# Kernel tuning notes

Measured on AMD Instinct MI355X. Metric: run time of the kernel, lower is better.

Reference implementation:

```python
import jax, jax.numpy as jnp
import numpy as np

N, D, NCLS = 1, 64, 21
R, C = 512, 512
R_IN, C_IN = 256, 256


def setup_inputs() -> dict:
    key = jax.random.key(0)
    k1, k2, k3 = jax.random.split(key, 3)
    # regular mesh with unit spacing -> grid_interval_X = grid_interval_Y = 1.0
    gy, gx = jnp.meshgrid(jnp.arange(R, dtype=jnp.float32),
                          jnp.arange(C, dtype=jnp.float32), indexing='ij')
    grid = jnp.stack([gy, gx], axis=-1)[None]  # [1,R,C,2]
    # float query coordinates inside the grid
    u = jax.random.uniform(k1, (N, R_IN, C_IN, 2), dtype=jnp.float32)
    grid_inte = u * jnp.array([R - 1.0, C - 1.0], dtype=jnp.float32)
    feat = jax.random.normal(k2, (N, D, R_IN, C_IN), dtype=jnp.float32)
    lbs = jax.random.uniform(k3, (N, NCLS, R, C), dtype=jnp.float32)
    wei = jnp.float32(1.0)
    return {"grid_inte": grid_inte, "grid": grid, "feat": feat, "lbs": lbs, "wei": wei}


def _forward(grid_inte, grid, feat, lbs, wei):
    n, r_in, c_in, _ = grid_inte.shape
    r, c = grid.shape[1], grid.shape[2]
    d = feat.shape[1]
    ncls = lbs.shape[1]
    M = r_in * c_in

    dx = grid[0, 2, 2, 0] - grid[0, 1, 2, 0]
    dy = grid[0, 2, 2, 1] - grid[0, 2, 1, 1]

    # bilinear upsample feat (half-pixel centers, matches torch align_corners=False)
    feat_grid = jax.image.resize(feat, (n, d, r, c), method='bilinear')
    feat_grid = feat_grid.reshape(d, r * c)              # N == 1

    # integer cell indices of each query (no grad, as in torch.no_grad())
    rp0 = jax.lax.stop_gradient(jnp.floor(grid_inte[..., 0] / dx)).astype(jnp.int32).reshape(-1)
    rp1 = jax.lax.stop_gradient(jnp.floor(grid_inte[..., 1] / dy)).astype(jnp.int32).reshape(-1)

    offs = jnp.arange(-2, 3, dtype=jnp.int32)
    oi, oj = jnp.meshgrid(offs, offs, indexing='ij')     # 5x5 neighborhood
    oi, oj = oi.reshape(-1), oj.reshape(-1)              # [25]
    rows = jnp.clip(rp0[None, :] + oi[:, None], 0, r - 1)  # [25, M]
    cols = jnp.clip(rp1[None, :] + oj[:, None], 0, c - 1)
    idx = rows * c + cols                                 # [25, M]

    fg = feat_grid[:, idx]                                # [D, 25, M] gather
    feat_flat = feat.reshape(d, M)
    # Gaussian-style affinity per tap: exp(-wei * mean_D (diff^2))
    dist = jnp.exp(-wei * jnp.mean((fg - feat_flat[:, None, :]) ** 2, axis=0))  # [25, M]

    lbs_flat = lbs.reshape(ncls, r * c)
    lg = lbs_flat[:, idx]                                 # [ncls, 25, M] gather
    voting = jnp.einsum('ctm,tm->cm', lg, dist)           # weighted label voting
    dist_sum = jnp.sum(dist, axis=0)                      # [M]
    out = voting / jnp.clip(dist_sum, 1e-15)[None, :]
    return out.reshape(n, ncls, r_in, c_in)


def reference(grid_inte, grid, feat, lbs, wei):
    return _forward(grid_inte, grid, feat, lbs, wei)
```

## Files before the change

### kernel.cpp

```cpp
#include <hip/hip_runtime.h>
#include <stdint.h>

#define M_TOT 65536
#define LBS_S 262144
#define REC   24

typedef _Float16 h2 __attribute__((ext_vector_type(2)));
typedef _Float16 h8 __attribute__((ext_vector_type(8)));
typedef float fx2 __attribute__((ext_vector_type(2)));
union H8 { h8 v; h2 h[4]; };

__device__ __forceinline__ int rfl(int v) { return __builtin_amdgcn_readfirstlane(v); }
__device__ __forceinline__ float bperm(int l, float v) {
  return __int_as_float(__builtin_amdgcn_ds_bpermute(l << 2, __float_as_int(v)));
}
__device__ __forceinline__ int bpermi(int l, int v) {
  return __builtin_amdgcn_ds_bpermute(l << 2, v);
}
__device__ __forceinline__ float merge2(float a, float b, bool hi, int xo) {
  const float keep = hi ? b : a;
  const float send = hi ? a : b;
  return keep + __shfl_xor(send, xo, 64);
}

#if __has_builtin(__builtin_amdgcn_fdot2)
__device__ __forceinline__ float fdot2(h2 a, h2 b, float c) {
  return __builtin_amdgcn_fdot2(a, b, c, false);
}
#else
__device__ __forceinline__ float fdot2(h2 a, h2 b, float c) {
  return fmaf((float)a.x, (float)b.x, fmaf((float)a.y, (float)b.y, c));
}
#endif

#if __has_builtin(__builtin_amdgcn_cvt_pk_f32_fp8) && __has_builtin(__builtin_amdgcn_cvt_pk_fp8_f32)
#define FP8_HW 1
#endif

__device__ __forceinline__ uint32_t enc1_sw(float x) {
  uint32_t b = __float_as_uint(x);
  const uint32_t s = b >> 31;
  uint32_t ax = b & 0x7fffffffu;
  if (ax > 0x43e00000u) ax = 0x43e00000u;
  const int e = (int)(ax >> 23) - 127;
  uint32_t out;
  if (e >= -6) {
    const uint32_t r = ax + 0x00080000u;
    const int e2 = (int)(r >> 23) - 127;
    if (e2 > 8) out = (15u << 3) | 6u;
    else out = ((uint32_t)(e2 + 7) << 3) | ((r >> 20) & 7u);
  } else if (e >= -10) {
    const float af = __uint_as_float(ax);
    int m = (int)(af * 512.0f + 0.5f);
    out = (m > 7) ? ((1u << 3) | 0u) : (uint32_t)m;
  } else {
    out = 0;
  }
  return out | (s << 7);
}
__device__ __forceinline__ float dec1_sw(uint32_t b) {
  const uint32_t e = (b >> 3) & 15u, m = b & 7u;
  float f;
  if (e) f = __uint_as_float(((e + 120u) << 23) | (m << 20));
  else f = (float)m * 0.001953125f;
  return (b & 0x80u) ? -f : f;
}

__device__ __forceinline__ uint32_t enc_pk4(float a, float b, float c, float d) {
#ifdef FP8_HW
  int r = __builtin_amdgcn_cvt_pk_fp8_f32(a, b, 0, false);
  r = __builtin_amdgcn_cvt_pk_fp8_f32(c, d, r, true);
  return (uint32_t)r;
#else
  return enc1_sw(a) | (enc1_sw(b) << 8) | (enc1_sw(c) << 16) | (enc1_sw(d) << 24);
#endif
}
__device__ __forceinline__ void dec_pk8(uint32_t lo, uint32_t hi, float* o) {
#ifdef FP8_HW
  const fx2 a = __builtin_amdgcn_cvt_pk_f32_fp8((int)lo, false);
  const fx2 b = __builtin_amdgcn_cvt_pk_f32_fp8((int)lo, true);
  const fx2 c = __builtin_amdgcn_cvt_pk_f32_fp8((int)hi, false);
  const fx2 d = __builtin_amdgcn_cvt_pk_f32_fp8((int)hi, true);
  o[0] = a.x; o[1] = a.y; o[2] = b.x; o[3] = b.y;
  o[4] = c.x; o[5] = c.y; o[6] = d.x; o[7] = d.y;
#else
  o[0] = dec1_sw(lo & 255); o[1] = dec1_sw((lo >> 8) & 255);
  o[2] = dec1_sw((lo >> 16) & 255); o[3] = dec1_sw(lo >> 24);
  o[4] = dec1_sw(hi & 255); o[5] = dec1_sw((hi >> 8) & 255);
  o[6] = dec1_sw((hi >> 16) & 255); o[7] = dec1_sw(hi >> 24);
#endif
}

__global__ __launch_bounds__(256) void k_prep(const float* __restrict__ feat,
                                              const float* __restrict__ lbs,
                                              _Float16* __restrict__ feat_h,
                                              uint8_t* __restrict__ feat_q,
                                              uint8_t* __restrict__ rec) {
  __shared__ float ldsf[64 * 65];
  const int l = threadIdx.x & 63;
  const int w = threadIdx.x >> 6;
  if (blockIdx.x < 1024) {
    float(*tile)[65] = (float(*)[65])ldsf;
    const int s0 = blockIdx.x * 64;
#pragma unroll
    for (int k = 0; k < 16; ++k) {
      const int d = w * 16 + k;
      tile[d][l] = feat[(size_t)d * M_TOT + s0 + l];
    }
    __syncthreads();
    const int lh = l & 31, hs = l >> 5;
    h2* out2 = (h2*)feat_h;
#pragma unroll
    for (int k = 0; k < 8; ++k) {
      const int s = w * 16 + 2 * k + hs;
      h2 v;
      v.x = (_Float16)tile[2 * lh][s];
      v.y = (_Float16)tile[2 * lh + 1][s];
      out2[(size_t)(s0 + s) * 32 + lh] = v;
    }
    uint2* outq = (uint2*)feat_q;
#pragma unroll
    for (int it = 0; it < 2; ++it) {
      const int s = w * 16 + it * 8 + (l >> 3);
      const int cb = l & 7;
      const float* col = &tile[8 * cb][s];
      uint2 u;
      u.x = enc_pk4(col[0 * 65], col[1 * 65], col[2 * 65], col[3 * 65]);
      u.y = enc_pk4(col[4 * 65], col[5 * 65], col[6 * 65], col[7 * 65]);
      outq[(size_t)(s0 + s) * 8 + cb] = u;
    }
  } else {
    uint8_t* buf = ((uint8_t*)ldsf) + w * (64 * REC);
    const int sb = (blockIdx.x - 1024) * 256 + w * 64;
#pragma unroll
    for (int c = 0; c < 21; ++c)
      buf[l * REC + 2 + c] = (uint8_t)(lbs[(size_t)c * LBS_S + sb + l] * 255.0f + 0.5f);
    __syncthreads();
    const uint32_t* src = (const uint32_t*)buf;
    uint32_t* dst = (uint32_t*)(rec + (size_t)sb * REC);
#pragma unroll
    for (int k = 0; k < 6; ++k) dst[k * 64 + l] = src[k * 64 + l];
  }
}

__global__ __launch_bounds__(256) void k_n2(const uint8_t* __restrict__ feat_q,
                                            uint8_t* __restrict__ rec) {
  const int lane = threadIdx.x & 63;
  const int cb = lane & 7;
  const int g = lane >> 3;
  const int quad = blockIdx.x * 32 + (int)(threadIdx.x >> 6) * 8 + g;
  const int a = quad >> 8;
  const int b = quad & 255;
  const int ra[3] = {max(a - 1, 0), a, min(a + 1, 255)};
  const int cbn[3] = {max(b - 1, 0), b, min(b + 1, 255)};

  const uint2* fq = (const uint2*)feat_q;
  float F[3][3][8];
#pragma unroll
  for (int i = 0; i < 3; ++i)
#pragma unroll
    for (int j = 0; j < 3; ++j) {
      const uint2 u = fq[(size_t)((ra[i] << 8) + cbn[j]) * 8 + cb];
      dec_pk8(u.x, u.y, F[i][j]);
    }

  float wye[2], wxe[2];
  int cye[2], cxe[2];
#pragma unroll
  for (int e = 0; e < 2; ++e) {
    const float yf = fminf(fmaxf((float)(2 * a + e) * 0.5f - 0.25f, 0.0f), 255.0f);
    const int y0 = min((int)yf, 254);
    wye[e] = yf - (float)y0;
    cye[e] = y0 - (a - 1);
    const float xf = fminf(fmaxf((float)(2 * b + e) * 0.5f - 0.25f, 0.0f), 255.0f);
    const int x0 = min((int)xf, 254);
    wxe[e] = xf - (float)x0;
    cxe[e] = x0 - (b - 1);
  }

  float colv[3][2][8];
#pragma unroll
  for (int r = 0; r < 3; ++r)
#pragma unroll
    for (int e = 0; e < 2; ++e) {
      const bool s1 = (cxe[e] == 1);
#pragma unroll
      for (int j = 0; j < 8; ++j) {
        const float A = s1 ? F[r][1][j] : F[r][0][j];
        const float B = s1 ? F[r][2][j] : F[r][1][j];
        colv[r][e][j] = fmaf(wxe[e], B - A, A);
      }
    }

  float sq[4];
#pragma unroll
  for (int ey = 0; ey < 2; ++ey)
#pragma unroll
    for (int ex = 0; ex < 2; ++ex) {
      const bool s1 = (cye[ey] == 1);
      float nn = 0.0f;
#pragma unroll
      for (int j = 0; j < 8; ++j) {
        const float A = s1 ? colv[1][ex][j] : colv[0][ex][j];
        const float B = s1 ? colv[2][ex][j] : colv[1][ex][j];
        const float v = fmaf(wye[ey], B - A, A);
        nn = fmaf(v, v, nn);
      }
      sq[ey * 2 + ex] = nn;
    }

  const bool b0 = lane & 1, b1 = lane & 2;
  float m0 = merge2(sq[0], sq[1], b0, 1);
  float m1 = merge2(sq[2], sq[3], b0, 1);
  float mm = merge2(m0, m1, b1, 2);
  mm += __shfl_xor(mm, 4, 64);
  if ((lane & 7) < 4) {
    const int ey = (lane >> 1) & 1, ex = lane & 1;
    *(_Float16*)(rec + (size_t)((2 * a + ey) * 512 + 2 * b + ex) * REC) = (_Float16)mm;
  }
}

__global__ __launch_bounds__(256) void k_main(const float* __restrict__ grid_inte,
                                              const float* __restrict__ grid,
                                              const _Float16* __restrict__ feat_h,
                                              const uint8_t* __restrict__ feat_q,
                                              const uint8_t* __restrict__ rec,
                                              const float* __restrict__ wei_p,
                                              float* __restrict__ out) {
  const int lane = threadIdx.x & 63;
  const int P = lane >> 5;
  const int m0 = rfl((int)blockIdx.x * 8 + (int)(threadIdx.x >> 6) * 2);
  const int m = m0 + P;

  const float dx = grid[(2 * 512 + 2) * 2 + 0] - grid[(1 * 512 + 2) * 2 + 0];
  const float dy = grid[(2 * 512 + 2) * 2 + 1] - grid[(2 * 512 + 1) * 2 + 1];
  const float wei = wei_p[0];

  const float gi0 = grid_inte[m * 2 + 0];
  const float gi1 = grid_inte[m * 2 + 1];
  const int rp0 = (int)floorf(gi0 / dx);
  const int rp1 = (int)floorf(gi1 / dy);
  const int by = (rp0 - 3) >> 1;
  const int bx = (rp1 - 3) >> 1;

  const int cb = lane & 7;
  const int g2 = (lane >> 3) & 3;
  const h8* fp = (const h8*)feat_h;
  const uint2* fq = (const uint2*)feat_q;

  H8 C;
  C.v = fp[(size_t)m * 8 + cb];
  uint2 pk[4];
  const int xx = min(max(bx + g2, 0), 255);
#pragma unroll
  for (int k = 0; k < 4; ++k) {
    const int yy = min(max(by + k, 0), 255);
    pk[k] = fq[(size_t)((yy << 8) + xx) * 8 + cb];
  }

  const int t = lane & 31;
  const int ti = (t * 13) >> 6;
  const int tj = t - 5 * ti;
  const int r5 = min(max(rp0 + ti - 2, 0), 511);
  const int c5 = min(max(rp1 + tj - 2, 0), 511);
  const float yf = fminf(fmaxf((float)r5 * 0.5f - 0.25f, 0.0f), 255.0f);
  const int y0 = min((int)yf, 254);
  const float wy = yf - (float)y0;
  const int qy = y0 - by;
  const float xf = fminf(fmaxf((float)c5 * 0.5f - 0.25f, 0.0f), 255.0f);
  const int x0 = min((int)xf, 254);
  const float wx = xf - (float)x0;
  const int qx = x0 - bx;
  const int lidx = r5 * 512 + c5;

  const float n2g = (float)*(const _Float16*)(rec + (size_t)lidx * REC);

  const int vg = (lane >= 42) ? 2 : ((lane >= 21) ? 1 : 0);
  const int cc = min(lane - 21 * vg, 20);
  float lg0[9];
#pragma unroll
  for (int it = 0; it < 9; ++it) {
    const int idxt = bpermi(3 * it + vg, lidx);
    lg0[it] = (float)rec[(size_t)idxt * REC + 2 + cc];
  }

  float cf[8];
#pragma unroll
  for (int q = 0; q < 4; ++q) {
    cf[2 * q] = (float)C.h[q].x;
    cf[2 * q + 1] = (float)C.h[q].y;
  }
  float nhp = 0.0f;
#pragma unroll
  for (int q = 0; q < 4; ++q) nhp = fdot2(C.h[q], C.h[q], nhp);
  nhp *= -0.5f;
  float pr[4];
#pragma unroll
  for (int k = 0; k < 4; ++k) {
    float pp[8];
    dec_pk8(pk[k].x, pk[k].y, pp);
    float acc = nhp;
#pragma unroll
    for (int j = 0; j < 8; ++j) acc = fmaf(pp[j], cf[j], acc);
    pr[k] = acc;
  }
  const bool hb0 = lane & 1, hb1 = lane & 2;
  float mm0 = merge2(pr[0], pr[1], hb0, 1);
  float mm1 = merge2(pr[2], pr[3], hb0, 1);
  float Dv = merge2(mm0, mm1, hb1, 2);
  Dv += __shfl_xor(Dv, 4, 64);

  const int pb = P << 5;
  const int s00 = qy * 4 + qx;
  const int s01 = s00 + 1, s10 = s00 + 4, s11 = s00 + 5;
  const int l00 = pb | ((s00 & 3) << 3) | (s00 >> 2);
  const int l01 = pb | ((s01 & 3) << 3) | (s01 >> 2);
  const int l10 = pb | ((s10 & 3) << 3) | (s10 >> 2);
  const int l11 = pb | ((s11 & 3) << 3) | (s11 >> 2);
  const float d00 = bperm(l00, Dv);
  const float d01 = bperm(l01, Dv);
  const float d10 = bperm(l10, Dv);
  const float d11 = bperm(l11, Dv);
  const float lo = fmaf(wx, d01 - d00, d00);
  const float hi = fmaf(wx, d11 - d10, d10);
  const float crossD = fmaf(wy, hi - lo, lo);

  const float mse = fmaf(-2.0f, crossD, n2g) * 0.015625f;
  float dist = __expf(-wei * mse);
  dist = (t < 25) ? dist : 0.0f;

  float lg1[9];
#pragma unroll
  for (int it = 0; it < 9; ++it) {
    const int idxt = bpermi(32 + 3 * it + vg, lidx);
    lg1[it] = (float)rec[(size_t)idxt * REC + 2 + cc];
  }

  float voteA = 0.0f, dsumA = 0.0f;
#pragma unroll
  for (int it = 0; it < 9; ++it) {
    const float dt = bperm(3 * it + vg, dist);
    voteA = fmaf(lg0[it], dt, voteA);
    dsumA += dt;
  }
  const float vA = voteA + bperm(lane + 21, voteA) + bperm(lane + 42, voteA);
  const float dA = dsumA + bperm(lane + 21, dsumA) + bperm(lane + 42, dsumA);

  float voteB = 0.0f, dsumB = 0.0f;
#pragma unroll
  for (int it = 0; it < 9; ++it) {
    const float dt = bperm(32 + 3 * it + vg, dist);
    voteB = fmaf(lg1[it], dt, voteB);
    dsumB += dt;
  }
  const float vB = voteB + bperm(lane + 21, voteB) + bperm(lane + 42, voteB);
  const float dB = dsumB + bperm(lane + 21, dsumB) + bperm(lane + 42, dsumB);

  const float s255 = 1.0f / 255.0f;
  if (lane < 21) {
    out[lane * M_TOT + m0]     = vA * s255 / fmaxf(dA, 1e-15f);
    out[lane * M_TOT + m0 + 1] = vB * s255 / fmaxf(dB, 1e-15f);
  }
}

extern "C" void kernel_launch(void* const* d_in, const int* in_sizes, int n_in,
                              void* d_out, int out_size, void* d_ws, size_t ws_size,
                              hipStream_t stream) {
  const float* grid_inte = (const float*)d_in[0];
  const float* grid      = (const float*)d_in[1];
  const float* feat      = (const float*)d_in[2];
  const float* lbs       = (const float*)d_in[3];
  const float* wei       = (const float*)d_in[4];
  float* out = (float*)d_out;

  char* ws = (char*)d_ws;
  _Float16* feat_h = (_Float16*)ws;
  uint8_t*  feat_q = (uint8_t*)(ws + 8388608);
  uint8_t*  rec    = (uint8_t*)(ws + 12582912);

  hipLaunchKernelGGL(k_prep, dim3(2048), dim3(256), 0, stream, feat, lbs, feat_h, feat_q, rec);
  hipLaunchKernelGGL(k_n2, dim3(M_TOT / 32), dim3(256), 0, stream, feat_q, rec);
  hipLaunchKernelGGL(k_main, dim3(M_TOT / 8), dim3(256), 0, stream,
                     grid_inte, grid, feat_h, feat_q, rec, wei, out);
}
```

Before: 50.78 us.

## Sort queries by spatial bin and use fp8 center features in main kernel

Adds a counting sort of query points into 16x16-cell spatial bins (histogram fused into k_n2, a single-block scan, and a scatter kernel), so k_main processes queries in spatially coherent order and its gathers from rec and feat_q hit cache better. It also drops the fp16 copy of feat and reads the center feature from the fp8 buffer, which cuts prep write traffic but lowers the precision of the center vector. In exchange it adds two kernel launches, global atomics, an indirection through order, and output writes scattered by query index.

```diff
diff --git a/kernel.cpp b/kernel.cpp
--- a/kernel.cpp
+++ b/kernel.cpp
@@ -3,12 +3,11 @@
 
 #define M_TOT 65536
 #define LBS_S 262144
+#define NBINS 1024
 #define REC   24
 
 typedef _Float16 h2 __attribute__((ext_vector_type(2)));
-typedef _Float16 h8 __attribute__((ext_vector_type(8)));
 typedef float fx2 __attribute__((ext_vector_type(2)));
-union H8 { h8 v; h2 h[4]; };
 
 __device__ __forceinline__ int rfl(int v) { return __builtin_amdgcn_readfirstlane(v); }
 __device__ __forceinline__ float bperm(int l, float v) {
@@ -22,16 +21,6 @@
   const float send = hi ? a : b;
   return keep + __shfl_xor(send, xo, 64);
 }
-
-#if __has_builtin(__builtin_amdgcn_fdot2)
-__device__ __forceinline__ float fdot2(h2 a, h2 b, float c) {
-  return __builtin_amdgcn_fdot2(a, b, c, false);
-}
-#else
-__device__ __forceinline__ float fdot2(h2 a, h2 b, float c) {
-  return fmaf((float)a.x, (float)b.x, fmaf((float)a.y, (float)b.y, c));
-}
-#endif
 
 #if __has_builtin(__builtin_amdgcn_cvt_pk_f32_fp8) && __has_builtin(__builtin_amdgcn_cvt_pk_fp8_f32)
 #define FP8_HW 1
@@ -91,14 +80,26 @@
 #endif
 }
 
+__device__ __forceinline__ int pixel_key(const float* grid_inte, const float* grid, int i) {
+  const float dx = grid[(2 * 512 + 2) * 2 + 0] - grid[(1 * 512 + 2) * 2 + 0];
+  const float dy = grid[(2 * 512 + 2) * 2 + 1] - grid[(2 * 512 + 1) * 2 + 1];
+  const int rp0 = (int)floorf(grid_inte[i * 2 + 0] / dx);
+  const int rp1 = (int)floorf(grid_inte[i * 2 + 1] / dy);
+  return ((rp0 >> 4) << 5) | (rp1 >> 4);
+}
+
 __global__ __launch_bounds__(256) void k_prep(const float* __restrict__ feat,
                                               const float* __restrict__ lbs,
-                                              _Float16* __restrict__ feat_h,
                                               uint8_t* __restrict__ feat_q,
-                                              uint8_t* __restrict__ rec) {
+                                              uint8_t* __restrict__ rec,
+                                              int* __restrict__ hist) {
   __shared__ float ldsf[64 * 65];
   const int l = threadIdx.x & 63;
   const int w = threadIdx.x >> 6;
+  if (blockIdx.x == 0) {
+#pragma unroll
+    for (int k = 0; k < 4; ++k) hist[k * 256 + threadIdx.x] = 0;
+  }
   if (blockIdx.x < 1024) {
     float(*tile)[65] = (float(*)[65])ldsf;
     const int s0 = blockIdx.x * 64;
@@ -108,16 +109,6 @@
       tile[d][l] = feat[(size_t)d * M_TOT + s0 + l];
     }
     __syncthreads();
-    const int lh = l & 31, hs = l >> 5;
-    h2* out2 = (h2*)feat_h;
-#pragma unroll
-    for (int k = 0; k < 8; ++k) {
-      const int s = w * 16 + 2 * k + hs;
-      h2 v;
-      v.x = (_Float16)tile[2 * lh][s];
-      v.y = (_Float16)tile[2 * lh + 1][s];
-      out2[(size_t)(s0 + s) * 32 + lh] = v;
-    }
     uint2* outq = (uint2*)feat_q;
 #pragma unroll
     for (int it = 0; it < 2; ++it) {
@@ -144,7 +135,14 @@
 }
 
 __global__ __launch_bounds__(256) void k_n2(const uint8_t* __restrict__ feat_q,
-                                            uint8_t* __restrict__ rec) {
+                                            uint8_t* __restrict__ rec,
+                                            const float* __restrict__ grid_inte,
+                                            const float* __restrict__ grid,
+                                            int* __restrict__ hist) {
+  if (blockIdx.x < 256) {
+    const int i = blockIdx.x * 256 + threadIdx.x;
+    atomicAdd(&hist[pixel_key(grid_inte, grid, i)], 1);
+  }
   const int lane = threadIdx.x & 63;
   const int cb = lane & 7;
   const int g = lane >> 3;
@@ -220,17 +218,49 @@
   }
 }
 
+__global__ __launch_bounds__(256) void k_scan(const int* __restrict__ hist,
+                                              int* __restrict__ cursor) {
+  __shared__ int wsum[4];
+  const int t = threadIdx.x;
+  const int4 h = ((const int4*)hist)[t];
+  const int s = h.x + h.y + h.z + h.w;
+  int sc = s;
+#pragma unroll
+  for (int o = 1; o < 64; o <<= 1) {
+    const int u = __shfl_up(sc, o, 64);
+    if ((t & 63) >= o) sc += u;
+  }
+  if ((t & 63) == 63) wsum[t >> 6] = sc;
+  __syncthreads();
+  int base = 0;
+  for (int wv = 0; wv < (t >> 6); ++wv) base += wsum[wv];
+  const int ex = base + sc - s;
+  cursor[4 * t + 0] = ex;
+  cursor[4 * t + 1] = ex + h.x;
+  cursor[4 * t + 2] = ex + h.x + h.y;
+  cursor[4 * t + 3] = ex + h.x + h.y + h.z;
+}
+
+__global__ __launch_bounds__(256) void k_scatter(const float* __restrict__ grid_inte,
+                                                 const float* __restrict__ grid,
+                                                 int* __restrict__ cursor,
+                                                 int* __restrict__ order) {
+  const int i = blockIdx.x * 256 + threadIdx.x;
+  const int pos = atomicAdd(&cursor[pixel_key(grid_inte, grid, i)], 1);
+  order[pos] = i;
+}
+
 __global__ __launch_bounds__(256) void k_main(const float* __restrict__ grid_inte,
                                               const float* __restrict__ grid,
-                                              const _Float16* __restrict__ feat_h,
                                               const uint8_t* __restrict__ feat_q,
                                               const uint8_t* __restrict__ rec,
                                               const float* __restrict__ wei_p,
+                                              const int* __restrict__ order,
                                               float* __restrict__ out) {
   const int lane = threadIdx.x & 63;
   const int P = lane >> 5;
-  const int m0 = rfl((int)blockIdx.x * 8 + (int)(threadIdx.x >> 6) * 2);
-  const int m = m0 + P;
+  const int pos = (int)blockIdx.x * 8 + (int)(threadIdx.x >> 6) * 2 + P;
+  const int m = order[pos];
 
   const float dx = grid[(2 * 512 + 2) * 2 + 0] - grid[(1 * 512 + 2) * 2 + 0];
   const float dy = grid[(2 * 512 + 2) * 2 + 1] - grid[(2 * 512 + 1) * 2 + 1];
@@ -245,11 +275,9 @@
 
   const int cb = lane & 7;
   const int g2 = (lane >> 3) & 3;
-  const h8* fp = (const h8*)feat_h;
   const uint2* fq = (const uint2*)feat_q;
 
-  H8 C;
-  C.v = fp[(size_t)m * 8 + cb];
+  const uint2 ck = fq[(size_t)m * 8 + cb];
   uint2 pk[4];
   const int xx = min(max(bx + g2, 0), 255);
 #pragma unroll
@@ -285,14 +313,10 @@
   }
 
   float cf[8];
-#pragma unroll
-  for (int q = 0; q < 4; ++q) {
-    cf[2 * q] = (float)C.h[q].x;
-    cf[2 * q + 1] = (float)C.h[q].y;
-  }
+  dec_pk8(ck.x, ck.y, cf);
   float nhp = 0.0f;
 #pragma unroll
-  for (int q = 0; q < 4; ++q) nhp = fdot2(C.h[q], C.h[q], nhp);
+  for (int j = 0; j < 8; ++j) nhp = fmaf(cf[j], cf[j], nhp);
   nhp *= -0.5f;
   float pr[4];
 #pragma unroll
@@ -356,10 +380,11 @@
   const float vB = voteB + bperm(lane + 21, voteB) + bperm(lane + 42, voteB);
   const float dB = dsumB + bperm(lane + 21, dsumB) + bperm(lane + 42, dsumB);
 
+  const int mB = bpermi(lane + 32, m);
   const float s255 = 1.0f / 255.0f;
   if (lane < 21) {
-    out[lane * M_TOT + m0]     = vA * s255 / fmaxf(dA, 1e-15f);
-    out[lane * M_TOT + m0 + 1] = vB * s255 / fmaxf(dB, 1e-15f);
+    out[lane * M_TOT + m]  = vA * s255 / fmaxf(dA, 1e-15f);
+    out[lane * M_TOT + mB] = vB * s255 / fmaxf(dB, 1e-15f);
   }
 }
 
@@ -374,12 +399,16 @@
   float* out = (float*)d_out;
 
   char* ws = (char*)d_ws;
-  _Float16* feat_h = (_Float16*)ws;
-  uint8_t*  feat_q = (uint8_t*)(ws + 8388608);
-  uint8_t*  rec    = (uint8_t*)(ws + 12582912);
-
-  hipLaunchKernelGGL(k_prep, dim3(2048), dim3(256), 0, stream, feat, lbs, feat_h, feat_q, rec);
-  hipLaunchKernelGGL(k_n2, dim3(M_TOT / 32), dim3(256), 0, stream, feat_q, rec);
+  uint8_t* feat_q = (uint8_t*)ws;
+  uint8_t* rec    = (uint8_t*)(ws + 4194304);
+  int*     order  = (int*)(ws + 10485760);
+  int*     hist   = (int*)(ws + 10747904);
+  int*     cursor = (int*)(ws + 10752000);
+
+  hipLaunchKernelGGL(k_prep, dim3(2048), dim3(256), 0, stream, feat, lbs, feat_q, rec, hist);
+  hipLaunchKernelGGL(k_n2, dim3(M_TOT / 32), dim3(256), 0, stream, feat_q, rec, grid_inte, grid, hist);
+  hipLaunchKernelGGL(k_scan, dim3(1), dim3(256), 0, stream, hist, cursor);
+  hipLaunchKernelGGL(k_scatter, dim3(M_TOT / 256), dim3(256), 0, stream, grid_inte, grid, cursor, order);
   hipLaunchKernelGGL(k_main, dim3(M_TOT / 8), dim3(256), 0, stream,
-                     grid_inte, grid, feat_h, feat_q, rec, wei, out);
-}
+                     grid_inte, grid, feat_q, rec, wei, order, out);
+}
```

New measurement: 81.97 us. +61.4%, slower.
